# Optimization experiments

Measured on AMD Instinct MI355X. Metric: run time of the kernel, lower is better.

The kernel has to match this reference:

```python
import jax, jax.numpy as jnp
import numpy as np

N_NODES = 100000
N_EDGES = 1600000
IN_F = 128
OUT_F = 64
BN_EPS = 1e-5


def setup_inputs() -> dict:
    key = jax.random.key(0)
    ks = jax.random.split(key, 6)
    feature = jax.random.normal(ks[0], (N_NODES, IN_F), dtype=jnp.float32)
    src = jax.random.randint(ks[1], (N_EDGES,), 0, N_NODES, dtype=jnp.int32)
    dst = jax.random.randint(ks[2], (N_EDGES,), 0, N_NODES, dtype=jnp.int32)
    W = jax.random.normal(ks[3], (IN_F, OUT_F), dtype=jnp.float32) * 0.05
    b = jnp.zeros((OUT_F,), dtype=jnp.float32)
    res_W = jax.random.normal(ks[4], (IN_F, OUT_F), dtype=jnp.float32) * 0.05
    res_b = jnp.zeros((OUT_F,), dtype=jnp.float32)
    gamma = jnp.ones((OUT_F,), dtype=jnp.float32)
    beta = jnp.zeros((OUT_F,), dtype=jnp.float32)
    return {"feature": feature, "src": src, "dst": dst, "W": W, "b": b,
            "res_W": res_W, "res_b": res_b, "gamma": gamma, "beta": beta,
            "idx": 0}


def _gcn_layer(feature, src, dst, W, b, res_W, res_b, gamma, beta):
    n = feature.shape[0]
    ones = jnp.ones_like(src, dtype=feature.dtype)
    # DGL norm='both': src-side uses out-degree, dst-side uses in-degree,
    # degrees clamped to min 1 (allow_zero_in_degree=True).
    out_deg = jax.ops.segment_sum(ones, src, num_segments=n)
    in_deg = jax.ops.segment_sum(ones, dst, num_segments=n)
    norm_src = jax.lax.rsqrt(jnp.maximum(out_deg, 1.0))  # [N]
    norm_dst = jax.lax.rsqrt(jnp.maximum(in_deg, 1.0))   # [N]

    # in_feats (128) > out_feats (64): DGL multiplies by W before aggregation.
    h = (feature * norm_src[:, None]) @ W                 # [N, OUT_F]
    agg = jax.ops.segment_sum(h[src], dst, num_segments=n)  # [N, OUT_F]
    conv = jax.nn.relu(agg * norm_dst[:, None] + b)

    # residual connection: activation(Linear(feature))
    res = jax.nn.relu(feature @ res_W + res_b)
    y = conv + res

    # BatchNorm1d (training mode, biased variance)
    mean = jnp.mean(y, axis=0)
    var = jnp.mean(jnp.square(y - mean), axis=0)
    y = (y - mean) * jax.lax.rsqrt(var + BN_EPS) * gamma + beta
    return y


def reference(feature, src, dst, W, b, res_W, res_b, gamma, beta, idx):
    # idx == 0 -> dropout branch is skipped (eval-deterministic reference)
    return _gcn_layer(feature, src, dst, W, b, res_W, res_b, gamma, beta)
```

## Files before the change

kernel.cpp:

```cpp
#include <hip/hip_runtime.h>
#include <hip/hip_fp16.h>

#define NCOL 64
#define KDIM 128
#define NB 512
#define CH 8192

typedef short bf16x8 __attribute__((ext_vector_type(8)));
typedef float f32x4 __attribute__((ext_vector_type(4)));
typedef float f32x2 __attribute__((ext_vector_type(2)));

__device__ __forceinline__ unsigned short f2bf(float f) {
    unsigned int u = __float_as_uint(f);
    return (unsigned short)((u + 0x7fffu + ((u >> 16) & 1u)) >> 16);
}
__device__ __forceinline__ float bflo(unsigned int u) { return __uint_as_float(u << 16); }
__device__ __forceinline__ float bfhi(unsigned int u) { return __uint_as_float(u & 0xffff0000u); }

__global__ __launch_bounds__(512) void hist_kernel(const int* __restrict__ dst,
                                                   int* __restrict__ bcnt,
                                                   int* __restrict__ gh, int E) {
    __shared__ int lh[NB];
    int tid = threadIdx.x;
    int c = blockIdx.x;
    if (tid < NB) lh[tid] = 0;
    __syncthreads();
    int c0 = c * CH;
    int cnt = min(CH, E - c0);
    for (int i = tid; i < cnt; i += 512)
        atomicAdd(&lh[dst[c0 + i] >> 8], 1);
    __syncthreads();
    if (tid < NB) {
        int v = lh[tid];
        gh[(size_t)c * NB + tid] = v;
        if (v) atomicAdd(&bcnt[tid], v);
    }
}

__global__ __launch_bounds__(256) void chunk_scan(int* __restrict__ gh,
                                                  const int* __restrict__ bcnt,
                                                  int* __restrict__ bbase,
                                                  int* __restrict__ row_start,
                                                  int nchunks, int N, int E) {
    __shared__ int wsum[4];
    __shared__ int red[4];
    __shared__ int carry_s, tot_s;
    int k = blockIdx.x;
    int tid = threadIdx.x, lane = tid & 63, wv = tid >> 6;

    int v = 0;
    if (tid < k) v = bcnt[tid];
    if (tid + 256 < k) v += bcnt[tid + 256];
#pragma unroll
    for (int off = 1; off < 64; off <<= 1) v += __shfl_xor(v, off);
    if (lane == 0) red[wv] = v;
    __syncthreads();
    if (tid == 0) {
        int base = red[0] + red[1] + red[2] + red[3];
        carry_s = base;
        bbase[k] = base;
        if (k == 0) row_start[N] = E;
    }
    __syncthreads();

    for (int t0 = 0; t0 < nchunks; t0 += 256) {
        int c = t0 + tid;
        int x = (c < nchunks) ? gh[(size_t)c * NB + k] : 0;
        int inc = x;
#pragma unroll
        for (int off = 1; off < 64; off <<= 1) {
            int t = __shfl_up(inc, off); if (lane >= off) inc += t;
        }
        if (lane == 63) wsum[wv] = inc;
        __syncthreads();
        if (tid == 0) {
            int run = 0;
            for (int i = 0; i < 4; ++i) { int t = wsum[i]; wsum[i] = run; run += t; }
            tot_s = run;
        }
        __syncthreads();
        int excl = carry_s + wsum[wv] + inc - x;
        if (c < nchunks) gh[(size_t)c * NB + k] = excl;
        __syncthreads();
        if (tid == 0) carry_s += tot_s;
        __syncthreads();
    }
}

__global__ __launch_bounds__(512) void scatter_pk(const int* __restrict__ src,
                                                  const int* __restrict__ dst,
                                                  const int* __restrict__ gh,
                                                  unsigned int* __restrict__ pk,
                                                  int* __restrict__ outcnt, int E) {
    __shared__ int lcur[NB];
    int tid = threadIdx.x;
    int c = blockIdx.x;
    if (tid < NB) lcur[tid] = gh[(size_t)c * NB + tid];
    __syncthreads();
    int c0 = c * CH;
    int cnt = min(CH, E - c0);
    for (int i = tid; i < cnt; i += 512) {
        int s = src[c0 + i], d = dst[c0 + i];
        atomicAdd(&outcnt[s], 1);
        int pos = atomicAdd(&lcur[d >> 8], 1);
        pk[pos] = ((unsigned)(d & 255) << 17) | (unsigned)s;
    }
}

__global__ __launch_bounds__(256) void fine_kernel(
    const unsigned int* __restrict__ pk, const int* __restrict__ bbase,
    int* __restrict__ row_start, int* __restrict__ ssrc, int E, int nbuck, int N) {
    __shared__ int hist[256];
    __shared__ int cur[256];
    __shared__ int wsum[4];
    int k = blockIdx.x;
    int tid = threadIdx.x, lane = tid & 63, wv = tid >> 6;
    int b0 = bbase[k];
    int b1 = (k + 1 < nbuck) ? bbase[k + 1] : E;

    hist[tid] = 0;
    __syncthreads();
    for (int i = b0 + tid; i < b1; i += 256)
        atomicAdd(&hist[pk[i] >> 17], 1);
    __syncthreads();

    int x = hist[tid], inc = x;
#pragma unroll
    for (int off = 1; off < 64; off <<= 1) {
        int t = __shfl_up(inc, off); if (lane >= off) inc += t;
    }
    if (lane == 63) wsum[wv] = inc;
    __syncthreads();
    if (tid == 0) { int run = 0; for (int i = 0; i < 4; ++i) { int t = wsum[i]; wsum[i] = run; run += t; } }
    __syncthreads();
    int excl = wsum[wv] + inc - x;

    int d = (k << 8) + tid;
    if (d < N) row_start[d] = b0 + excl;
    cur[tid] = b0 + excl;
    __syncthreads();

    for (int i = b0 + tid; i < b1; i += 256) {
        unsigned int p = pk[i];
        int pos = atomicAdd(&cur[p >> 17], 1);
        ssrc[pos] = (int)(p & 0x1FFFFu);
    }
}

__global__ __launch_bounds__(256) void matmul_mfma(
    const float* __restrict__ feat, const float* __restrict__ W,
    const float* __restrict__ RW, const float* __restrict__ res_b,
    const int* __restrict__ outcnt,
    unsigned int* __restrict__ hb8, unsigned int* __restrict__ r8, int N) {
    __shared__ bf16x8 Bf[2048];
    int tid = threadIdx.x;
    for (int idx = tid; idx < 2048; idx += 256) {
        int mat = idx >> 10;
        int kc = (idx >> 8) & 3;
        int ct = (idx >> 6) & 3;
        int l = idx & 63;
        const float* Wp = mat ? RW : W;
        int kbase = kc * 32 + (l >> 4) * 8;
        int col = ct * 16 + (l & 15);
        bf16x8 t;
#pragma unroll
        for (int j = 0; j < 8; ++j)
            t[j] = (short)f2bf(Wp[(size_t)(kbase + j) * NCOL + col]);
        Bf[idx] = t;
    }
    __syncthreads();

    int lane = tid & 63;
    int wid = tid >> 6;
    int ntiles = (N + 15) >> 4;
    int tile = blockIdx.x * 4 + wid;
    if (tile >= ntiles) return;
    int c16 = lane & 15, kg = lane >> 4;

    float rbv[4];
#pragma unroll
    for (int ct = 0; ct < 4; ++ct) rbv[ct] = res_b[ct * 16 + c16];

    int tb = tile << 4;
    f32x4 acch[4], accr[4];
#pragma unroll
    for (int ct = 0; ct < 4; ++ct) {
        acch[ct] = (f32x4){0.f, 0.f, 0.f, 0.f};
        accr[ct] = (f32x4){0.f, 0.f, 0.f, 0.f};
    }

    int arow = tb + c16; if (arow >= N) arow = N - 1;
    const float* fp = feat + (size_t)arow * KDIM + kg * 8;
#pragma unroll
    for (int kc = 0; kc < 4; ++kc) {
        float4 a0 = *(const float4*)(fp + kc * 32);
        float4 a1 = *(const float4*)(fp + kc * 32 + 4);
        bf16x8 af;
        af[0] = (short)f2bf(a0.x); af[1] = (short)f2bf(a0.y);
        af[2] = (short)f2bf(a0.z); af[3] = (short)f2bf(a0.w);
        af[4] = (short)f2bf(a1.x); af[5] = (short)f2bf(a1.y);
        af[6] = (short)f2bf(a1.z); af[7] = (short)f2bf(a1.w);
#pragma unroll
        for (int ct = 0; ct < 4; ++ct) {
            acch[ct] = __builtin_amdgcn_mfma_f32_16x16x32_bf16(
                af, Bf[(kc * 4 + ct) * 64 + lane], acch[ct], 0, 0, 0);
            accr[ct] = __builtin_amdgcn_mfma_f32_16x16x32_bf16(
                af, Bf[1024 + (kc * 4 + ct) * 64 + lane], accr[ct], 0, 0, 0);
        }
    }

    float nrm[4];
#pragma unroll
    for (int r = 0; r < 4; ++r) {
        int rw = tb + kg * 4 + r; if (rw >= N) rw = N - 1;
        nrm[r] = rsqrtf(fmaxf((float)outcnt[rw], 1.0f));
    }
#pragma unroll
    for (int r = 0; r < 4; ++r) {
        int row = tb + kg * 4 + r;
        if (row < N) {
            unsigned int p = 0;
            p = (unsigned int)__builtin_amdgcn_cvt_pk_fp8_f32(
                    acch[0][r] * nrm[r], acch[1][r] * nrm[r], (int)p, false);
            p = (unsigned int)__builtin_amdgcn_cvt_pk_fp8_f32(
                    acch[2][r] * nrm[r], acch[3][r] * nrm[r], (int)p, true);
            hb8[(size_t)row * 16 + c16] = p;
            float q0 = fmaxf(accr[0][r] + rbv[0], 0.0f);
            float q1 = fmaxf(accr[1][r] + rbv[1], 0.0f);
            float q2 = fmaxf(accr[2][r] + rbv[2], 0.0f);
            float q3 = fmaxf(accr[3][r] + rbv[3], 0.0f);
            r8[(size_t)row * 32 + c16]      = ((unsigned)f2bf(q1) << 16) | f2bf(q0);
            r8[(size_t)row * 32 + 16 + c16] = ((unsigned)f2bf(q3) << 16) | f2bf(q2);
        }
    }
}

#define GATHER_ROW_STEP(eBase, eEnd, A0, A1, A2, A3)                                   \
    {                                                                                   \
        int e0 = (eBase) + e4, e1 = e0 + 4, e2 = e0 + 8, e3 = e0 + 12;                  \
        int i0 = (e0 < (eEnd)) ? ssrc[e0] : -1;                                         \
        int i1 = (e1 < (eEnd)) ? ssrc[e1] : -1;                                         \
        int i2 = (e2 < (eEnd)) ? ssrc[e2] : -1;                                         \
        int i3 = (e3 < (eEnd)) ? ssrc[e3] : -1;                                         \
        unsigned int v0 = (i0 >= 0) ? hb8[(size_t)i0 * 16 + dw] : 0u;                   \
        unsigned int v1 = (i1 >= 0) ? hb8[(size_t)i1 * 16 + dw] : 0u;                   \
        unsigned int v2 = (i2 >= 0) ? hb8[(size_t)i2 * 16 + dw] : 0u;                   \
        unsigned int v3 = (i3 >= 0) ? hb8[(size_t)i3 * 16 + dw] : 0u;                   \
        f32x2 l0 = __builtin_amdgcn_cvt_pk_f32_fp8((int)v0, false);                     \
        f32x2 h0 = __builtin_amdgcn_cvt_pk_f32_fp8((int)v0, true);                      \
        f32x2 l1 = __builtin_amdgcn_cvt_pk_f32_fp8((int)v1, false);                     \
        f32x2 h1 = __builtin_amdgcn_cvt_pk_f32_fp8((int)v1, true);                      \
        f32x2 l2 = __builtin_amdgcn_cvt_pk_f32_fp8((int)v2, false);                     \
        f32x2 h2 = __builtin_amdgcn_cvt_pk_f32_fp8((int)v2, true);                      \
        f32x2 l3 = __builtin_amdgcn_cvt_pk_f32_fp8((int)v3, false);                     \
        f32x2 h3 = __builtin_amdgcn_cvt_pk_f32_fp8((int)v3, true);                      \
        A0 += (l0[0] + l1[0]) + (l2[0] + l3[0]);                                        \
        A1 += (l0[1] + l1[1]) + (l2[1] + l3[1]);                                        \
        A2 += (h0[0] + h1[0]) + (h2[0] + h3[0]);                                        \
        A3 += (h0[1] + h1[1]) + (h2[1] + h3[1]);                                        \
    }

__global__ __launch_bounds__(256) void gather_kernel(
    const int* __restrict__ row_start, const int* __restrict__ ssrc,
    const unsigned int* __restrict__ hb8, const unsigned int* __restrict__ r8,
    const float* __restrict__ b,
    float* __restrict__ y, float* __restrict__ stats, int N) {
    int tid = threadIdx.x, lane = tid & 63, wid = tid >> 6;
    int e4 = lane >> 4, dw = lane & 15;
    int rowSel = e4 >> 1, ch = e4 & 1;
    int colLo = (ch << 5) + dw;
    int wave = blockIdx.x * 4 + wid;
    int nwaves = gridDim.x * 4;

    float bcLo = b[colLo], bcHi = b[colLo + 16];
    float bnLo = 0.f, bnHi = 0.f, bnsqLo = 0.f, bnsqHi = 0.f;

    for (int d0 = wave * 2; d0 < N; d0 += 2 * nwaves) {
        int d1 = d0 + 1;
        int a0 = row_start[d0], a1 = row_start[d0 + 1];
        int b0e = 0, b1e = 0;
        if (d1 < N) { b0e = a1; b1e = row_start[d1 + 1]; }

        float A0 = 0.f, A1 = 0.f, A2 = 0.f, A3 = 0.f;
        float B0 = 0.f, B1 = 0.f, B2 = 0.f, B3 = 0.f;
        int nit = max((a1 - a0 + 15) >> 4, (b1e - b0e + 15) >> 4);
        for (int it = 0; it < nit; ++it) {
            GATHER_ROW_STEP(a0 + it * 16, a1, A0, A1, A2, A3)
            GATHER_ROW_STEP(b0e + it * 16, b1e, B0, B1, B2, B3)
        }

#pragma unroll
        for (int off = 16; off <= 32; off <<= 1) {
            A0 += __shfl_xor(A0, off); A1 += __shfl_xor(A1, off);
            A2 += __shfl_xor(A2, off); A3 += __shfl_xor(A3, off);
            B0 += __shfl_xor(B0, off); B1 += __shfl_xor(B1, off);
            B2 += __shfl_xor(B2, off); B3 += __shfl_xor(B3, off);
        }

        int dd = d0 + rowSel;
        if (dd < N) {
            int deg = rowSel ? (b1e - b0e) : (a1 - a0);
            float nd = rsqrtf(fmaxf((float)deg, 1.0f));
            float vLo = rowSel ? (ch ? B2 : B0) : (ch ? A2 : A0);
            float vHi = rowSel ? (ch ? B3 : B1) : (ch ? A3 : A1);
            unsigned int rr = r8[(size_t)dd * 32 + ch * 16 + dw];
            float v0 = fmaxf(vLo * nd + bcLo, 0.f) + bflo(rr);
            float v1 = fmaxf(vHi * nd + bcHi, 0.f) + bfhi(rr);
            float* yp = &y[(size_t)dd * NCOL + colLo];
            yp[0] = v0;
            yp[16] = v1;
            bnLo += v0; bnsqLo += v0 * v0;
            bnHi += v1; bnsqHi += v1 * v1;
        }
    }

    bnLo += __shfl_xor(bnLo, 32); bnsqLo += __shfl_xor(bnsqLo, 32);
    bnHi += __shfl_xor(bnHi, 32); bnsqHi += __shfl_xor(bnsqHi, 32);

    __shared__ float bnred[4][128];
    if (lane < 32) {
        bnred[wid][colLo] = bnLo;
        bnred[wid][colLo + 16] = bnHi;
        bnred[wid][64 + colLo] = bnsqLo;
        bnred[wid][64 + colLo + 16] = bnsqHi;
    }
    __syncthreads();
    if (tid < 128) {
        float v = bnred[0][tid] + bnred[1][tid] + bnred[2][tid] + bnred[3][tid];
        unsafeAtomicAdd(&stats[tid], v);
    }
}

__global__ __launch_bounds__(256) void apply_kernel(float* __restrict__ y,
                                                    const float* __restrict__ stats,
                                                    const float* __restrict__ gamma,
                                                    const float* __restrict__ beta,
                                                    float invN, int total4) {
    __shared__ float sc[64], sh[64];
    int tid = threadIdx.x;
    if (tid < 64) {
        float mean = stats[tid] * invN;
        float var = stats[64 + tid] * invN - mean * mean;
        float s = gamma[tid] * rsqrtf(var + 1e-5f);
        sc[tid] = s;
        sh[tid] = beta[tid] - mean * s;
    }
    __syncthreads();
    int i = blockIdx.x * blockDim.x + tid;
    int stride = gridDim.x * blockDim.x;
    float4* y4 = (float4*)y;
    for (; i < total4; i += stride) {
        float4 v = y4[i];
        int cbase = (i & 15) << 2;
        float4 s = *(const float4*)&sc[cbase];
        float4 t = *(const float4*)&sh[cbase];
        v.x = v.x * s.x + t.x;
        v.y = v.y * s.y + t.y;
        v.z = v.z * s.z + t.z;
        v.w = v.w * s.w + t.w;
        y4[i] = v;
    }
}

extern "C" void kernel_launch(void* const* d_in, const int* in_sizes, int n_in,
                              void* d_out, int out_size, void* d_ws, size_t ws_size,
                              hipStream_t stream) {
    const float* feat  = (const float*)d_in[0];
    const int*   src   = (const int*)d_in[1];
    const int*   dst   = (const int*)d_in[2];
    const float* W     = (const float*)d_in[3];
    const float* b     = (const float*)d_in[4];
    const float* RW    = (const float*)d_in[5];
    const float* rb    = (const float*)d_in[6];
    const float* gamma = (const float*)d_in[7];
    const float* beta  = (const float*)d_in[8];

    int N = in_sizes[0] / KDIM;
    int E = in_sizes[1];
    float* out = (float*)d_out;
    int nbuck = (N + 255) >> 8;
    int nchunks = (E + CH - 1) / CH;

    char* wsb = (char*)d_ws;
    unsigned int* hb8 = (unsigned int*)wsb;                wsb += (size_t)N * 16 * 4;
    unsigned int* r8  = (unsigned int*)wsb;                wsb += (size_t)N * 32 * 4;
    unsigned int* pk  = (unsigned int*)wsb;                wsb += (size_t)E * 4;
    int*   ssrc     = (int*)wsb;                           wsb += (size_t)E * 4;
    int*   row_start= (int*)wsb;                           wsb += (size_t)(N + 1) * 4;
    int*   outcnt   = (int*)wsb;                           wsb += (size_t)N * 4;
    float* stats    = (float*)wsb;                         wsb += 256 * 4;
    int*   bcnt     = (int*)wsb;                           wsb += NB * 4;
    int*   bbase    = (int*)wsb;                           wsb += NB * 4;
    int*   gh       = (int*)wsb;

    hipMemsetAsync(outcnt, 0, ((size_t)N + 256 + NB) * 4, stream);

    hist_kernel<<<nchunks, 512, 0, stream>>>(dst, bcnt, gh, E);
    chunk_scan<<<NB, 256, 0, stream>>>(gh, bcnt, bbase, row_start, nchunks, N, E);
    scatter_pk<<<nchunks, 512, 0, stream>>>(src, dst, gh, pk, outcnt, E);
    matmul_mfma<<<(((N + 15) >> 4) + 3) / 4, 256, 0, stream>>>(feat, W, RW, rb, outcnt, hb8, r8, N);
    fine_kernel<<<nbuck, 256, 0, stream>>>(pk, bbase, row_start, ssrc, E, nbuck, N);
    gather_kernel<<<2048, 256, 0, stream>>>(row_start, ssrc, hb8, r8, b, out, stats, N);
    apply_kernel<<<2048, 256, 0, stream>>>(out, stats, gamma, beta, 1.0f / (float)N, (N * NCOL) / 4);
}
```

Before: 228.5 us.

## Fuse gather and batchnorm apply via cooperative grid sync with register caching

Replaces the separate gather and batchnorm-apply kernels with one cooperative kernel. Each thread keeps up to 13 row-pair results in registers, then after a grid-wide sync on the accumulated statistics it writes normalized values directly. This removes the write-then-reread of the output and one kernel launch. In exchange it uses more registers, limits the grid to the co-resident block count, and adds the cost of a grid barrier. It falls back to the old two-kernel path if the cooperative launch fails.

```diff
diff --git a/kernel.cpp b/kernel.cpp
--- a/kernel.cpp
+++ b/kernel.cpp
@@ -1,10 +1,15 @@
 #include <hip/hip_runtime.h>
 #include <hip/hip_fp16.h>
+#include <hip/hip_cooperative_groups.h>
+
+namespace cg = cooperative_groups;
 
 #define NCOL 64
 #define KDIM 128
 #define NB 512
 #define CH 8192
+#define GBLK_MAX 1024
+#define GMAX 13
 
 typedef short bf16x8 __attribute__((ext_vector_type(8)));
 typedef float f32x4 __attribute__((ext_vector_type(4)));
@@ -260,6 +265,45 @@
         A3 += (h0[1] + h1[1]) + (h2[1] + h3[1]);                                        \
     }
 
+__device__ __forceinline__ int gather_pair(
+    const int* __restrict__ row_start, const int* __restrict__ ssrc,
+    const unsigned int* __restrict__ hb8, const unsigned int* __restrict__ r8,
+    float bcLo, float bcHi, int d0, int N,
+    int e4, int dw, int rowSel, int ch, int colLo,
+    float& v0o, float& v1o) {
+    int d1 = d0 + 1;
+    int a0 = row_start[d0], a1 = row_start[d0 + 1];
+    int b0e = 0, b1e = 0;
+    if (d1 < N) { b0e = a1; b1e = row_start[d1 + 1]; }
+
+    float A0 = 0.f, A1 = 0.f, A2 = 0.f, A3 = 0.f;
+    float B0 = 0.f, B1 = 0.f, B2 = 0.f, B3 = 0.f;
+    int nit = max((a1 - a0 + 15) >> 4, (b1e - b0e + 15) >> 4);
+    for (int it = 0; it < nit; ++it) {
+        GATHER_ROW_STEP(a0 + it * 16, a1, A0, A1, A2, A3)
+        GATHER_ROW_STEP(b0e + it * 16, b1e, B0, B1, B2, B3)
+    }
+
+#pragma unroll
+    for (int off = 16; off <= 32; off <<= 1) {
+        A0 += __shfl_xor(A0, off); A1 += __shfl_xor(A1, off);
+        A2 += __shfl_xor(A2, off); A3 += __shfl_xor(A3, off);
+        B0 += __shfl_xor(B0, off); B1 += __shfl_xor(B1, off);
+        B2 += __shfl_xor(B2, off); B3 += __shfl_xor(B3, off);
+    }
+
+    int dd = d0 + rowSel;
+    if (dd >= N) return -1;
+    int deg = rowSel ? (b1e - b0e) : (a1 - a0);
+    float nd = rsqrtf(fmaxf((float)deg, 1.0f));
+    float vLo = rowSel ? (ch ? B2 : B0) : (ch ? A2 : A0);
+    float vHi = rowSel ? (ch ? B3 : B1) : (ch ? A3 : A1);
+    unsigned int rr = r8[(size_t)dd * 32 + ch * 16 + dw];
+    v0o = fmaxf(vLo * nd + bcLo, 0.f) + bflo(rr);
+    v1o = fmaxf(vHi * nd + bcHi, 0.f) + bfhi(rr);
+    return dd;
+}
+
 __global__ __launch_bounds__(256) void gather_kernel(
     const int* __restrict__ row_start, const int* __restrict__ ssrc,
     const unsigned int* __restrict__ hb8, const unsigned int* __restrict__ r8,
@@ -276,36 +320,10 @@
     float bnLo = 0.f, bnHi = 0.f, bnsqLo = 0.f, bnsqHi = 0.f;
 
     for (int d0 = wave * 2; d0 < N; d0 += 2 * nwaves) {
-        int d1 = d0 + 1;
-        int a0 = row_start[d0], a1 = row_start[d0 + 1];
-        int b0e = 0, b1e = 0;
-        if (d1 < N) { b0e = a1; b1e = row_start[d1 + 1]; }
-
-        float A0 = 0.f, A1 = 0.f, A2 = 0.f, A3 = 0.f;
-        float B0 = 0.f, B1 = 0.f, B2 = 0.f, B3 = 0.f;
-        int nit = max((a1 - a0 + 15) >> 4, (b1e - b0e + 15) >> 4);
-        for (int it = 0; it < nit; ++it) {
-            GATHER_ROW_STEP(a0 + it * 16, a1, A0, A1, A2, A3)
-            GATHER_ROW_STEP(b0e + it * 16, b1e, B0, B1, B2, B3)
-        }
-
-#pragma unroll
-        for (int off = 16; off <= 32; off <<= 1) {
-            A0 += __shfl_xor(A0, off); A1 += __shfl_xor(A1, off);
-            A2 += __shfl_xor(A2, off); A3 += __shfl_xor(A3, off);
-            B0 += __shfl_xor(B0, off); B1 += __shfl_xor(B1, off);
-            B2 += __shfl_xor(B2, off); B3 += __shfl_xor(B3, off);
-        }
-
-        int dd = d0 + rowSel;
-        if (dd < N) {
-            int deg = rowSel ? (b1e - b0e) : (a1 - a0);
-            float nd = rsqrtf(fmaxf((float)deg, 1.0f));
-            float vLo = rowSel ? (ch ? B2 : B0) : (ch ? A2 : A0);
-            float vHi = rowSel ? (ch ? B3 : B1) : (ch ? A3 : A1);
-            unsigned int rr = r8[(size_t)dd * 32 + ch * 16 + dw];
-            float v0 = fmaxf(vLo * nd + bcLo, 0.f) + bflo(rr);
-            float v1 = fmaxf(vHi * nd + bcHi, 0.f) + bfhi(rr);
+        float v0, v1;
+        int dd = gather_pair(row_start, ssrc, hb8, r8, bcLo, bcHi,
+                             d0, N, e4, dw, rowSel, ch, colLo, v0, v1);
+        if (dd >= 0) {
             float* yp = &y[(size_t)dd * NCOL + colLo];
             yp[0] = v0;
             yp[16] = v1;
@@ -362,6 +380,102 @@
     }
 }
 
+__global__ __launch_bounds__(256, 4) void gather_fused(
+    const int* __restrict__ row_start, const int* __restrict__ ssrc,
+    const unsigned int* __restrict__ hb8, const unsigned int* __restrict__ r8,
+    const float* __restrict__ b, const float* __restrict__ gamma,
+    const float* __restrict__ beta,
+    float* __restrict__ y, float* __restrict__ stats, int N, float invN) {
+    int tid = threadIdx.x, lane = tid & 63, wid = tid >> 6;
+    int e4 = lane >> 4, dw = lane & 15;
+    int rowSel = e4 >> 1, ch = e4 & 1;
+    int colLo = (ch << 5) + dw;
+    int wave = blockIdx.x * 4 + wid;
+    int nwaves = gridDim.x * 4;
+    int stride = 2 * nwaves;
+
+    float bcLo = b[colLo], bcHi = b[colLo + 16];
+    float bnLo = 0.f, bnHi = 0.f, bnsqLo = 0.f, bnsqHi = 0.f;
+    float sv0[GMAX], sv1[GMAX];
+#pragma unroll
+    for (int k = 0; k < GMAX; ++k) { sv0[k] = 0.f; sv1[k] = 0.f; }
+
+#pragma unroll
+    for (int k = 0; k < GMAX; ++k) {
+        int d0 = wave * 2 + k * stride;
+        if (d0 < N) {
+            float v0, v1;
+            int dd = gather_pair(row_start, ssrc, hb8, r8, bcLo, bcHi,
+                                 d0, N, e4, dw, rowSel, ch, colLo, v0, v1);
+            if (dd >= 0) {
+                sv0[k] = v0; sv1[k] = v1;
+                bnLo += v0; bnsqLo += v0 * v0;
+                bnHi += v1; bnsqHi += v1 * v1;
+            }
+        }
+    }
+    for (int d0 = wave * 2 + GMAX * stride; d0 < N; d0 += stride) {
+        float v0, v1;
+        int dd = gather_pair(row_start, ssrc, hb8, r8, bcLo, bcHi,
+                             d0, N, e4, dw, rowSel, ch, colLo, v0, v1);
+        if (dd >= 0) {
+            float* yp = &y[(size_t)dd * NCOL + colLo];
+            yp[0] = v0; yp[16] = v1;
+            bnLo += v0; bnsqLo += v0 * v0;
+            bnHi += v1; bnsqHi += v1 * v1;
+        }
+    }
+
+    bnLo += __shfl_xor(bnLo, 32); bnsqLo += __shfl_xor(bnsqLo, 32);
+    bnHi += __shfl_xor(bnHi, 32); bnsqHi += __shfl_xor(bnsqHi, 32);
+
+    __shared__ float bnred[4][128];
+    if (lane < 32) {
+        bnred[wid][colLo] = bnLo;
+        bnred[wid][colLo + 16] = bnHi;
+        bnred[wid][64 + colLo] = bnsqLo;
+        bnred[wid][64 + colLo + 16] = bnsqHi;
+    }
+    __syncthreads();
+    if (tid < 128) {
+        float v = bnred[0][tid] + bnred[1][tid] + bnred[2][tid] + bnred[3][tid];
+        unsafeAtomicAdd(&stats[tid], v);
+    }
+
+    cg::this_grid().sync();
+
+    __shared__ float sc[64], sh[64];
+    if (tid < 64) {
+        float mean = stats[tid] * invN;
+        float var = stats[64 + tid] * invN - mean * mean;
+        float s = gamma[tid] * rsqrtf(var + 1e-5f);
+        sc[tid] = s;
+        sh[tid] = beta[tid] - mean * s;
+    }
+    __syncthreads();
+    float scLo = sc[colLo], shLo = sh[colLo];
+    float scHi = sc[colLo + 16], shHi = sh[colLo + 16];
+
+#pragma unroll
+    for (int k = 0; k < GMAX; ++k) {
+        int d0 = wave * 2 + k * stride;
+        int dd = d0 + rowSel;
+        if (d0 < N && dd < N) {
+            float* yp = &y[(size_t)dd * NCOL + colLo];
+            yp[0]  = sv0[k] * scLo + shLo;
+            yp[16] = sv1[k] * scHi + shHi;
+        }
+    }
+    for (int d0 = wave * 2 + GMAX * stride; d0 < N; d0 += stride) {
+        int dd = d0 + rowSel;
+        if (dd < N) {
+            float* yp = &y[(size_t)dd * NCOL + colLo];
+            yp[0]  = yp[0] * scLo + shLo;
+            yp[16] = yp[16] * scHi + shHi;
+        }
+    }
+}
+
 extern "C" void kernel_launch(void* const* d_in, const int* in_sizes, int n_in,
                               void* d_out, int out_size, void* d_ws, size_t ws_size,
                               hipStream_t stream) {
@@ -400,6 +514,28 @@
     scatter_pk<<<nchunks, 512, 0, stream>>>(src, dst, gh, pk, outcnt, E);
     matmul_mfma<<<(((N + 15) >> 4) + 3) / 4, 256, 0, stream>>>(feat, W, RW, rb, outcnt, hb8, r8, N);
     fine_kernel<<<nbuck, 256, 0, stream>>>(pk, bbase, row_start, ssrc, E, nbuck, N);
-    gather_kernel<<<2048, 256, 0, stream>>>(row_start, ssrc, hb8, r8, b, out, stats, N);
-    apply_kernel<<<2048, 256, 0, stream>>>(out, stats, gamma, beta, 1.0f / (float)N, (N * NCOL) / 4);
-}
+
+    float invN = 1.0f / (float)N;
+
+    int blocksPerCU = 0;
+    hipError_t qerr = hipOccupancyMaxActiveBlocksPerMultiprocessor(
+        &blocksPerCU, (const void*)gather_fused, 256, 0);
+    int coopGrid = 0;
+    if (qerr == hipSuccess && blocksPerCU > 0)
+        coopGrid = min(GBLK_MAX, blocksPerCU * 256);
+
+    bool fused_ok = false;
+    if (coopGrid >= 256) {
+        void* args[] = {(void*)&row_start, (void*)&ssrc, (void*)&hb8, (void*)&r8,
+                        (void*)&b, (void*)&gamma, (void*)&beta,
+                        (void*)&out, (void*)&stats, (void*)&N, (void*)&invN};
+        hipError_t cerr = hipLaunchCooperativeKernel((void*)gather_fused,
+                                                     dim3(coopGrid), dim3(256),
+                                                     args, 0, stream);
+        fused_ok = (cerr == hipSuccess);
+    }
+    if (!fused_ok) {
+        gather_kernel<<<2048, 256, 0, stream>>>(row_start, ssrc, hb8, r8, b, out, stats, N);
+        apply_kernel<<<2048, 256, 0, stream>>>(out, stats, gamma, beta, invN, (N * NCOL) / 4);
+    }
+}
```

Measured after the change: 278.7 us. 22.0% more time.
